# Optimization experiments

Measured on AMD Instinct MI355X. Metric: run time of the kernel, lower is better.

Reference implementation:

```python
import jax, jax.numpy as jnp
import numpy as np

B = 16384
OUT = 128          # output_size (per conditioning frame)
NCOND = 3
HID = 32           # MLP3 hidden
LSTM_H = 64        # lstm_output_size (input == hidden)
NPRED = 25
EPS = 1e-5


def setup_inputs() -> dict:
    key = jax.random.key(0)
    ks = jax.random.split(key, 20)
    d = {
        "x0": jax.random.normal(ks[0], (B, OUT), jnp.float32),
        "x1": jax.random.normal(ks[1], (B, OUT), jnp.float32),
        "x2": jax.random.normal(ks[2], (B, OUT), jnp.float32),
        # MLP3: Linear(384->32), BN, ReLU, Linear(32->32), BN, ReLU, Linear(32->64)
        "W1": jax.random.normal(ks[3], (HID, OUT * NCOND), jnp.float32) * 0.05,
        "b1": jnp.full((HID,), 0.03, jnp.float32),
        "g1": jnp.ones((HID,), jnp.float32),
        "beta1": jnp.zeros((HID,), jnp.float32),
        "W2": jax.random.normal(ks[4], (HID, HID), jnp.float32) * 0.1,
        "b2": jnp.full((HID,), 0.03, jnp.float32),
        "g2": jnp.ones((HID,), jnp.float32),
        "beta2": jnp.zeros((HID,), jnp.float32),
        "W3": jax.random.normal(ks[5], (LSTM_H, HID), jnp.float32) * 0.1,
        "b3": jnp.full((LSTM_H,), 0.03, jnp.float32),
        # LSTM (torch gate order i,f,g,o): weight_ih (4H,H), weight_hh (4H,H)
        "Wih": jax.random.normal(ks[6], (4 * LSTM_H, LSTM_H), jnp.float32) * 0.08,
        "Whh": jax.random.normal(ks[7], (4 * LSTM_H, LSTM_H), jnp.float32) * 0.08,
        "bih": jnp.zeros((4 * LSTM_H,), jnp.float32),
        "bhh": jnp.zeros((4 * LSTM_H,), jnp.float32),
    }
    return d


def _bn_train(h, g, b):
    # BatchNorm1d in training mode: biased batch statistics
    m = jnp.mean(h, axis=0)
    v = jnp.var(h, axis=0)
    return g * (h - m) * jax.lax.rsqrt(v + EPS) + b


def _lstm_step(inp, h, c, Wih, Whh, bih, bhh):
    gates = inp @ Wih.T + bih + h @ Whh.T + bhh  # (B, 4H)
    i, f, g, o = jnp.split(gates, 4, axis=1)
    c_new = jax.nn.sigmoid(f) * c + jax.nn.sigmoid(i) * jnp.tanh(g)
    h_new = jax.nn.sigmoid(o) * jnp.tanh(c_new)
    return h_new, c_new


def reference(x0, x1, x2, W1, b1, g1, beta1, W2, b2, g2, beta2, W3, b3,
              Wih, Whh, bih, bhh):
    x = jnp.concatenate([x0, x1, x2], axis=1)          # (B, 384)
    h = jax.nn.relu(_bn_train(x @ W1.T + b1, g1, beta1))
    h = jax.nn.relu(_bn_train(h @ W2.T + b2, g2, beta2))
    m = h @ W3.T + b3                                   # (B, 64)

    h0 = jnp.zeros((m.shape[0], LSTM_H), m.dtype)
    c0 = jnp.zeros_like(h0)
    # initial conditioning step (output discarded except as state/next input)
    h1, c1 = _lstm_step(m, h0, c0, Wih, Whh, bih, bhh)

    def step(carry, _):
        hh, cc = carry
        # loop feeds previous output back as input; output == h for 1-layer LSTM
        hn, cn = _lstm_step(hh, hh, cc, Wih, Whh, bih, bhh)
        return (hn, cn), hn

    _, outs = jax.lax.scan(step, (h1, c1), None, length=NPRED)  # (25, B, 64)
    return jnp.transpose(outs, (1, 0, 2))                        # (B, 25, 64)
```

## Files before the change

### kernel.cpp

```cpp
#include <hip/hip_runtime.h>


#define EPSV 1e-5f
#define LOG2E 1.4426950408889634f
#define K2    2.8853900817779268f

typedef __attribute__((ext_vector_type(8))) short bf16x8;
typedef __attribute__((ext_vector_type(4))) float f32x4;

__device__ __forceinline__ float rcp_f(float x) { return __builtin_amdgcn_rcpf(x); }
__device__ __forceinline__ void split_bf16(float x, ushort& hi, ushort& lo) {
    unsigned xb = __builtin_bit_cast(unsigned, x);
    hi = (ushort)(xb >> 16);
    float hif = __builtin_bit_cast(float, xb & 0xffff0000u);
    unsigned lb = __builtin_bit_cast(unsigned, x - hif);
    lo = (ushort)(lb >> 16);
}

__global__ __launch_bounds__(256) void k_prep(
    const float* __restrict__ Wih, const float* __restrict__ Whh,
    const float* __restrict__ bih, const float* __restrict__ bhh,
    const float* __restrict__ W1, const float* __restrict__ W2,
    ushort* __restrict__ Wih_hi, ushort* __restrict__ Wih_lo,
    ushort* __restrict__ Wsum_hi, ushort* __restrict__ Wsum_lo,
    ushort* __restrict__ W1hi, ushort* __restrict__ W1lo,
    ushort* __restrict__ W2hi, ushort* __restrict__ W2lo,
    float* __restrict__ bsum)
{
    int i = blockIdx.x * 256 + threadIdx.x;
    ushort h, l;
    if (i < 16384) {
        int j = i >> 6;
        float sc = (j >= 128 && j < 192) ? K2 : LOG2E;
        float wi  = Wih[i] * sc;
        float wsv = (Wih[i] + Whh[i]) * sc;
        split_bf16(wi, h, l);  Wih_hi[i] = h;  Wih_lo[i] = l;
        split_bf16(wsv, h, l); Wsum_hi[i] = h; Wsum_lo[i] = l;
    }
    if (i < 12288) { split_bf16(W1[i], h, l); W1hi[i] = h; W1lo[i] = l; }
    if (i < 1024)  { split_bf16(W2[i], h, l); W2hi[i] = h; W2lo[i] = l; }
    if (i < 256) {
        float sc = (i >= 128 && i < 192) ? K2 : LOG2E;
        bsum[i] = (bih[i] + bhh[i]) * sc;
    }
}

__global__ __launch_bounds__(256) void k_red(const float* __restrict__ part,
                                             const float* __restrict__ g,
                                             const float* __restrict__ be,
                                             float* __restrict__ scsh) {
    __shared__ float rs[256], rq[256];
    const int ch = blockIdx.x, t = threadIdx.x;
    float s = (part[t * 32 + ch] + part[(t + 256) * 32 + ch]) +
              (part[(t + 512) * 32 + ch] + part[(t + 768) * 32 + ch]);
    float q = (part[32768 + t * 32 + ch] + part[32768 + (t + 256) * 32 + ch]) +
              (part[32768 + (t + 512) * 32 + ch] + part[32768 + (t + 768) * 32 + ch]);
    rs[t] = s; rq[t] = q;
    __syncthreads();
    #pragma unroll
    for (int off = 128; off > 0; off >>= 1) {
        if (t < off) { rs[t] += rs[t + off]; rq[t] += rq[t + off]; }
        __syncthreads();
    }
    if (t == 0) {
        float mu = rs[0] * (1.f / 16384.f);
        float va = rq[0] * (1.f / 16384.f) - mu * mu;
        float sc = g[ch] * rsqrtf(va + EPSV);
        scsh[ch] = sc; scsh[32 + ch] = be[ch] - mu * sc;
    }
}

__global__ __launch_bounds__(256) void k_mlp1(
    const float* __restrict__ x0, const float* __restrict__ x1, const float* __restrict__ x2,
    const ushort* __restrict__ W1hi, const ushort* __restrict__ W1lo,
    const float* __restrict__ b1,
    float* __restrict__ pre, float* __restrict__ st1p)
{
    __shared__ __align__(16) ushort xhi[32 * 392];
    __shared__ __align__(16) ushort xlo[32 * 392];
    const int tid = threadIdx.x;
    const int r0  = blockIdx.x * 32;

    for (int a = 0; a < 3; ++a) {
        const float* xp = (a == 0) ? x0 : (a == 1) ? x1 : x2;
        const float4* src = (const float4*)(xp + (size_t)r0 * 128);
        #pragma unroll
        for (int it = 0; it < 4; ++it) {
            int i = it * 256 + tid;
            int row = i >> 5, c4 = i & 31;
            float4 v = src[i];
            ushort h0, l0, h1, l1, h2, l2, h3, l3;
            split_bf16(v.x, h0, l0); split_bf16(v.y, h1, l1);
            split_bf16(v.z, h2, l2); split_bf16(v.w, h3, l3);
            int ofs = row * 392 + a * 128 + c4 * 4;
            *(ushort4*)&xhi[ofs] = make_ushort4(h0, h1, h2, h3);
            *(ushort4*)&xlo[ofs] = make_ushort4(l0, l1, l2, l3);
        }
    }
    __syncthreads();

    const int lane = tid & 63, l15 = lane & 15, lg = lane >> 4, q = tid >> 6;
    const int m0 = (q & 1) * 16, n0 = (q >> 1) * 16;
    const float bias = b1[n0 + l15];
    f32x4 acc = {bias, bias, bias, bias};
    #pragma unroll
    for (int kt = 0; kt < 12; ++kt) {
        bf16x8 ahi = *(const bf16x8*)&xhi[(m0 + l15) * 392 + kt * 32 + lg * 8];
        bf16x8 alo = *(const bf16x8*)&xlo[(m0 + l15) * 392 + kt * 32 + lg * 8];
        bf16x8 bhi = *(const bf16x8*)(W1hi + (size_t)(n0 + l15) * 384 + kt * 32 + lg * 8);
        bf16x8 blo = *(const bf16x8*)(W1lo + (size_t)(n0 + l15) * 384 + kt * 32 + lg * 8);
        acc = __builtin_amdgcn_mfma_f32_16x16x32_bf16(ahi, bhi, acc, 0, 0, 0);
        acc = __builtin_amdgcn_mfma_f32_16x16x32_bf16(ahi, blo, acc, 0, 0, 0);
        acc = __builtin_amdgcn_mfma_f32_16x16x32_bf16(alo, bhi, acc, 0, 0, 0);
    }
    #pragma unroll
    for (int rg = 0; rg < 4; ++rg)
        pre[(size_t)(r0 + m0 + lg * 4 + rg) * 32 + n0 + l15] = acc[rg];
    float s  = (acc[0] + acc[1]) + (acc[2] + acc[3]);
    float sq = (acc[0] * acc[0] + acc[1] * acc[1]) + (acc[2] * acc[2] + acc[3] * acc[3]);
    s  += __shfl_xor(s, 16);  s  += __shfl_xor(s, 32);
    sq += __shfl_xor(sq, 16); sq += __shfl_xor(sq, 32);
    if (lg == 0) {
        int slot = (blockIdx.x * 2 + (q & 1)) * 32 + n0 + l15;
        st1p[slot] = s;
        st1p[32768 + slot] = sq;
    }
}

__global__ __launch_bounds__(256) void k_mlp2(
    float* __restrict__ pre, const float* __restrict__ scsh1,
    const ushort* __restrict__ W2hi, const ushort* __restrict__ W2lo,
    const float* __restrict__ b2, float* __restrict__ st2p)
{
    __shared__ __align__(16) ushort hhi[32 * 40];
    __shared__ __align__(16) ushort hlo[32 * 40];
    __shared__ float bnsc[32], bnsh[32];
    const int tid = threadIdx.x;
    const int r0  = blockIdx.x * 32;

    if (tid < 32) { bnsc[tid] = scsh1[tid]; bnsh[tid] = scsh1[32 + tid]; }
    __syncthreads();
    {
        int row = tid >> 3, c4 = tid & 7;
        float4 v = ((const float4*)(pre + (size_t)r0 * 32))[tid];
        float e0 = fmaxf(fmaf(v.x, bnsc[c4 * 4 + 0], bnsh[c4 * 4 + 0]), 0.f);
        float e1 = fmaxf(fmaf(v.y, bnsc[c4 * 4 + 1], bnsh[c4 * 4 + 1]), 0.f);
        float e2 = fmaxf(fmaf(v.z, bnsc[c4 * 4 + 2], bnsh[c4 * 4 + 2]), 0.f);
        float e3 = fmaxf(fmaf(v.w, bnsc[c4 * 4 + 3], bnsh[c4 * 4 + 3]), 0.f);
        ushort h0, l0, h1, l1, h2, l2, h3, l3;
        split_bf16(e0, h0, l0); split_bf16(e1, h1, l1);
        split_bf16(e2, h2, l2); split_bf16(e3, h3, l3);
        int ofs = row * 40 + c4 * 4;
        *(ushort4*)&hhi[ofs] = make_ushort4(h0, h1, h2, h3);
        *(ushort4*)&hlo[ofs] = make_ushort4(l0, l1, l2, l3);
    }
    __syncthreads();

    const int lane = tid & 63, l15 = lane & 15, lg = lane >> 4, q = tid >> 6;
    const int m0 = (q & 1) * 16, n0 = (q >> 1) * 16;
    const float bias = b2[n0 + l15];
    f32x4 acc = {bias, bias, bias, bias};
    bf16x8 ahi = *(const bf16x8*)&hhi[(m0 + l15) * 40 + lg * 8];
    bf16x8 alo = *(const bf16x8*)&hlo[(m0 + l15) * 40 + lg * 8];
    bf16x8 bhi = *(const bf16x8*)(W2hi + (size_t)(n0 + l15) * 32 + lg * 8);
    bf16x8 blo = *(const bf16x8*)(W2lo + (size_t)(n0 + l15) * 32 + lg * 8);
    acc = __builtin_amdgcn_mfma_f32_16x16x32_bf16(ahi, bhi, acc, 0, 0, 0);
    acc = __builtin_amdgcn_mfma_f32_16x16x32_bf16(ahi, blo, acc, 0, 0, 0);
    acc = __builtin_amdgcn_mfma_f32_16x16x32_bf16(alo, bhi, acc, 0, 0, 0);

    #pragma unroll
    for (int rg = 0; rg < 4; ++rg)
        pre[(size_t)(r0 + m0 + lg * 4 + rg) * 32 + n0 + l15] = acc[rg];
    float s  = (acc[0] + acc[1]) + (acc[2] + acc[3]);
    float sq = (acc[0] * acc[0] + acc[1] * acc[1]) + (acc[2] * acc[2] + acc[3] * acc[3]);
    s  += __shfl_xor(s, 16);  s  += __shfl_xor(s, 32);
    sq += __shfl_xor(sq, 16); sq += __shfl_xor(sq, 32);
    if (lg == 0) {
        int slot = (blockIdx.x * 2 + (q & 1)) * 32 + n0 + l15;
        st2p[slot] = s;
        st2p[32768 + slot] = sq;
    }
}

__global__ __launch_bounds__(256, 2) void k_lstm(
    const float* __restrict__ pre, const float* __restrict__ scsh2,
    const float* __restrict__ W3, const float* __restrict__ b3,
    const ushort* __restrict__ Wih_hi, const ushort* __restrict__ Wih_lo,
    const ushort* __restrict__ Wsum_hi, const ushort* __restrict__ Wsum_lo,
    const float* __restrict__ bsum, float* __restrict__ out)
{
    __shared__ __align__(16) ushort hhi[2][2][16][72];
    __shared__ __align__(16) ushort hlo[2][2][16][72];
    __shared__ float bn2sc[32], bn2sh[32];
    const int tid  = threadIdx.x;
    const int lane = tid & 63, l15 = lane & 15, lg = lane >> 4, q = tid >> 6;
    const int r0   = blockIdx.x * 32;

    if (tid < 32) { bn2sc[tid] = scsh2[tid]; bn2sh[tid] = scsh2[32 + tid]; }
    __syncthreads();

    {
        const int row = tid & 31, seg = tid >> 5;
        float h2[32];
        const float4* pr = (const float4*)(pre + (size_t)(r0 + row) * 32);
        #pragma unroll
        for (int j4 = 0; j4 < 8; ++j4) {
            float4 v = pr[j4];
            h2[j4 * 4 + 0] = v.x; h2[j4 * 4 + 1] = v.y;
            h2[j4 * 4 + 2] = v.z; h2[j4 * 4 + 3] = v.w;
        }
        #pragma unroll
        for (int j = 0; j < 32; ++j) h2[j] = fmaxf(fmaf(h2[j], bn2sc[j], bn2sh[j]), 0.f);
        #pragma unroll
        for (int uu = 0; uu < 8; ++uu) {
            int u = seg * 8 + uu;
            const float* w = W3 + u * 32;
            float a0 = 0.f, a1 = 0.f, a2 = 0.f, a3 = 0.f;
            #pragma unroll
            for (int k = 0; k < 32; k += 4) {
                a0 = fmaf(h2[k + 0], w[k + 0], a0);
                a1 = fmaf(h2[k + 1], w[k + 1], a1);
                a2 = fmaf(h2[k + 2], w[k + 2], a2);
                a3 = fmaf(h2[k + 3], w[k + 3], a3);
            }
            float m = b3[u] + ((a0 + a1) + (a2 + a3));
            ushort mh, ml; split_bf16(m, mh, ml);
            hhi[row >> 4][0][row & 15][u] = mh;
            hlo[row >> 4][0][row & 15][u] = ml;
        }
    }

    float bias[4];
    #pragma unroll
    for (int nt = 0; nt < 4; ++nt) bias[nt] = bsum[nt * 64 + q * 16 + l15];
    float cA[4] = {0.f, 0.f, 0.f, 0.f}, cB[4] = {0.f, 0.f, 0.f, 0.f};

    float* obA[4];
    float* obB[4];
    #pragma unroll
    for (int rg = 0; rg < 4; ++rg) {
        obA[rg] = out + (size_t)(r0 + lg * 4 + rg) * 1600 + (q * 16 + l15);
        obB[rg] = out + (size_t)(r0 + 16 + lg * 4 + rg) * 1600 + (q * 16 + l15);
    }

    bf16x8 Bhi[4][2], Blo[4][2];
    const size_t wofs = (size_t)(q * 16 + l15) * 64 + lg * 8;
    #pragma unroll
    for (int nt = 0; nt < 4; ++nt)
        #pragma unroll
        for (int kt = 0; kt < 2; ++kt) {
            Bhi[nt][kt] = *(const bf16x8*)(Wih_hi + (size_t)nt * 4096 + wofs + kt * 32);
            Blo[nt][kt] = *(const bf16x8*)(Wih_lo + (size_t)nt * 4096 + wofs + kt * 32);
        }
    __syncthreads();

#define MFMA_GATES(ACC, G, BUF)                                                  \
    {                                                                            \
        _Pragma("unroll")                                                        \
        for (int nt = 0; nt < 4; ++nt)                                           \
            ACC[nt] = (f32x4){bias[nt], bias[nt], bias[nt], bias[nt]};           \
        _Pragma("unroll")                                                        \
        for (int kt = 0; kt < 2; ++kt) {                                         \
            bf16x8 ahi = *(const bf16x8*)&hhi[G][BUF][l15][kt * 32 + lg * 8];    \
            bf16x8 alo = *(const bf16x8*)&hlo[G][BUF][l15][kt * 32 + lg * 8];    \
            _Pragma("unroll")                                                    \
            for (int nt = 0; nt < 4; ++nt) {                                     \
                ACC[nt] = __builtin_amdgcn_mfma_f32_16x16x32_bf16(ahi, Bhi[nt][kt], ACC[nt], 0, 0, 0); \
                ACC[nt] = __builtin_amdgcn_mfma_f32_16x16x32_bf16(ahi, Blo[nt][kt], ACC[nt], 0, 0, 0); \
                ACC[nt] = __builtin_amdgcn_mfma_f32_16x16x32_bf16(alo, Bhi[nt][kt], ACC[nt], 0, 0, 0); \
            }                                                                    \
        }                                                                        \
    }

#define ACT(ACC, C, G, WBUF, OB, SLOT, WRST)                                     \
    {                                                                            \
        const int u = q * 16 + l15;                                              \
        _Pragma("unroll")                                                        \
        for (int rg = 0; rg < 4; ++rg) {                                         \
            int row = lg * 4 + rg;                                               \
            float iv = ACC[0][rg], fv = ACC[1][rg];                              \
            float gv = ACC[2][rg], ov = ACC[3][rg];                              \
            float Af = __builtin_amdgcn_exp2f(-fv);                              \
            float Ai = __builtin_amdgcn_exp2f(-iv);                              \
            float Bg = __builtin_amdgcn_exp2f(gv);                               \
            float sig = (Bg - 1.f) * rcp_f((1.f + Ai) * (Bg + 1.f));             \
            float cc = C[rg] * rcp_f(1.f + Af) + sig;                            \
            C[rg] = cc;                                                          \
            float Ao = __builtin_amdgcn_exp2f(-ov);                              \
            float C2 = __builtin_amdgcn_exp2f(cc * K2);                          \
            float hn = (C2 - 1.f) * rcp_f((1.f + Ao) * (C2 + 1.f));              \
            ushort hh, hl; split_bf16(hn, hh, hl);                               \
            hhi[G][WBUF][row][u] = hh;                                           \
            hlo[G][WBUF][row][u] = hl;                                           \
            if (WRST)                                                            \
                OB[rg][(size_t)(SLOT) * 64] = hn;                                \
        }                                                                        \
    }

    f32x4 accA[4], accB[4];

    MFMA_GATES(accA, 0, 0);
    MFMA_GATES(accB, 1, 0);
    #pragma unroll
    for (int nt = 0; nt < 4; ++nt)
        #pragma unroll
        for (int kt = 0; kt < 2; ++kt) {
            Bhi[nt][kt] = *(const bf16x8*)(Wsum_hi + (size_t)nt * 4096 + wofs + kt * 32);
            Blo[nt][kt] = *(const bf16x8*)(Wsum_lo + (size_t)nt * 4096 + wofs + kt * 32);
        }
    ACT(accA, cA, 0, 1, obA, 0, 0);
    ACT(accB, cB, 1, 1, obB, 0, 0);
    __syncthreads();

    #pragma unroll 1
    for (int s = 1; s <= 25; ++s) {
        const int rb = s & 1, wb = rb ^ 1;
        MFMA_GATES(accA, 0, rb);
        MFMA_GATES(accB, 1, rb);
        ACT(accA, cA, 0, wb, obA, s - 1, 1);
        ACT(accB, cB, 1, wb, obB, s - 1, 1);
        __syncthreads();
    }

#undef MFMA_GATES
#undef ACT
}

extern "C" void kernel_launch(void* const* d_in, const int* in_sizes, int n_in,
                              void* d_out, int out_size, void* d_ws, size_t ws_size,
                              hipStream_t stream) {
    const float* x0   = (const float*)d_in[0];
    const float* x1   = (const float*)d_in[1];
    const float* x2   = (const float*)d_in[2];
    const float* W1   = (const float*)d_in[3];
    const float* b1   = (const float*)d_in[4];
    const float* g1   = (const float*)d_in[5];
    const float* be1  = (const float*)d_in[6];
    const float* W2   = (const float*)d_in[7];
    const float* b2   = (const float*)d_in[8];
    const float* g2   = (const float*)d_in[9];
    const float* be2  = (const float*)d_in[10];
    const float* W3   = (const float*)d_in[11];
    const float* b3   = (const float*)d_in[12];
    const float* Wih  = (const float*)d_in[13];
    const float* Whh  = (const float*)d_in[14];
    const float* bih  = (const float*)d_in[15];
    const float* bhh  = (const float*)d_in[16];

    float* ws    = (float*)d_ws;
    float* pre   = ws;
    float* st1p  = ws + 524288;
    float* st2p  = ws + 589824;
    float* scsh1 = ws + 655360;
    float* scsh2 = ws + 655424;
    float* bsum  = ws + 655488;
    ushort* ub   = (ushort*)(ws + 655744);
    ushort* Wih_hi  = ub;
    ushort* Wih_lo  = ub + 16384;
    ushort* Wsum_hi = ub + 32768;
    ushort* Wsum_lo = ub + 49152;
    ushort* W1hi    = ub + 65536;
    ushort* W1lo    = ub + 77824;
    ushort* W2hi    = ub + 90112;
    ushort* W2lo    = ub + 91136;

    hipLaunchKernelGGL(k_prep, dim3(64), dim3(256), 0, stream,
                       Wih, Whh, bih, bhh, W1, W2,
                       Wih_hi, Wih_lo, Wsum_hi, Wsum_lo, W1hi, W1lo, W2hi, W2lo, bsum);
    hipLaunchKernelGGL(k_mlp1, dim3(512), dim3(256), 0, stream,
                       x0, x1, x2, W1hi, W1lo, b1, pre, st1p);
    hipLaunchKernelGGL(k_red, dim3(32), dim3(256), 0, stream, st1p, g1, be1, scsh1);
    hipLaunchKernelGGL(k_mlp2, dim3(512), dim3(256), 0, stream,
                       pre, scsh1, W2hi, W2lo, b2, st2p);
    hipLaunchKernelGGL(k_red, dim3(32), dim3(256), 0, stream, st2p, g2, be2, scsh2);
    hipLaunchKernelGGL(k_lstm, dim3(512), dim3(256), 0, stream,
                       pre, scsh2, W3, b3,
                       Wih_hi, Wih_lo, Wsum_hi, Wsum_lo, bsum, (float*)d_out);
}
```

Measured before the change: 87.45 us.

## Eliminate prep kernel: split MLP weights in-kernel, fold LSTM prep into reduction

Removes the standalone weight-prep launch. k_mlp1 and k_mlp2 now load the fp32 W1/W2 directly and split them into bf16 hi/lo register fragments inside each block. The LSTM weight split moves into the first k_red launch. k_mlp1 also gets a launch bound of 2 waves per SIMD. Separately, k_lstm makes the upper half of its blocks s_sleep once before the recurrence, apparently to stagger memory or issue contention. The trade is one fewer launch against redundant per-block splitting of W1, higher register pressure, and a deliberate stall in half the LSTM blocks.

```diff
diff --git a/kernel.cpp b/kernel.cpp
--- a/kernel.cpp
+++ b/kernel.cpp
@@ -16,41 +16,45 @@
     unsigned lb = __builtin_bit_cast(unsigned, x - hif);
     lo = (ushort)(lb >> 16);
 }
-
-__global__ __launch_bounds__(256) void k_prep(
+__device__ __forceinline__ void split8(const float* w, bf16x8& hiv, bf16x8& lov) {
+    ushort hs[8], ls[8];
+    #pragma unroll
+    for (int j = 0; j < 8; ++j) split_bf16(w[j], hs[j], ls[j]);
+    hiv = *(bf16x8*)hs;
+    lov = *(bf16x8*)ls;
+}
+
+__global__ __launch_bounds__(256) void k_red(
+    const float* __restrict__ part, const float* __restrict__ g,
+    const float* __restrict__ be, float* __restrict__ scsh,
+    int do_prep,
     const float* __restrict__ Wih, const float* __restrict__ Whh,
     const float* __restrict__ bih, const float* __restrict__ bhh,
-    const float* __restrict__ W1, const float* __restrict__ W2,
     ushort* __restrict__ Wih_hi, ushort* __restrict__ Wih_lo,
     ushort* __restrict__ Wsum_hi, ushort* __restrict__ Wsum_lo,
-    ushort* __restrict__ W1hi, ushort* __restrict__ W1lo,
-    ushort* __restrict__ W2hi, ushort* __restrict__ W2lo,
     float* __restrict__ bsum)
 {
-    int i = blockIdx.x * 256 + threadIdx.x;
-    ushort h, l;
-    if (i < 16384) {
-        int j = i >> 6;
-        float sc = (j >= 128 && j < 192) ? K2 : LOG2E;
-        float wi  = Wih[i] * sc;
-        float wsv = (Wih[i] + Whh[i]) * sc;
-        split_bf16(wi, h, l);  Wih_hi[i] = h;  Wih_lo[i] = l;
-        split_bf16(wsv, h, l); Wsum_hi[i] = h; Wsum_lo[i] = l;
-    }
-    if (i < 12288) { split_bf16(W1[i], h, l); W1hi[i] = h; W1lo[i] = l; }
-    if (i < 1024)  { split_bf16(W2[i], h, l); W2hi[i] = h; W2lo[i] = l; }
-    if (i < 256) {
-        float sc = (i >= 128 && i < 192) ? K2 : LOG2E;
-        bsum[i] = (bih[i] + bhh[i]) * sc;
-    }
-}
-
-__global__ __launch_bounds__(256) void k_red(const float* __restrict__ part,
-                                             const float* __restrict__ g,
-                                             const float* __restrict__ be,
-                                             float* __restrict__ scsh) {
     __shared__ float rs[256], rq[256];
     const int ch = blockIdx.x, t = threadIdx.x;
+
+    if (do_prep) {
+        #pragma unroll
+        for (int e = 0; e < 2; ++e) {
+            int i = blockIdx.x * 512 + e * 256 + t;
+            int j = i >> 6;
+            float sc = (j >= 128 && j < 192) ? K2 : LOG2E;
+            float wi  = Wih[i] * sc;
+            float wsv = (Wih[i] + Whh[i]) * sc;
+            ushort h, l;
+            split_bf16(wi, h, l);  Wih_hi[i] = h;  Wih_lo[i] = l;
+            split_bf16(wsv, h, l); Wsum_hi[i] = h; Wsum_lo[i] = l;
+        }
+        if (blockIdx.x == 0) {
+            float sc = (t >= 128 && t < 192) ? K2 : LOG2E;
+            bsum[t] = (bih[t] + bhh[t]) * sc;
+        }
+    }
+
     float s = (part[t * 32 + ch] + part[(t + 256) * 32 + ch]) +
               (part[(t + 512) * 32 + ch] + part[(t + 768) * 32 + ch]);
     float q = (part[32768 + t * 32 + ch] + part[32768 + (t + 256) * 32 + ch]) +
@@ -70,16 +74,31 @@
     }
 }
 
-__global__ __launch_bounds__(256) void k_mlp1(
+__global__ __launch_bounds__(256, 2) void k_mlp1(
     const float* __restrict__ x0, const float* __restrict__ x1, const float* __restrict__ x2,
-    const ushort* __restrict__ W1hi, const ushort* __restrict__ W1lo,
-    const float* __restrict__ b1,
+    const float* __restrict__ W1, const float* __restrict__ b1,
     float* __restrict__ pre, float* __restrict__ st1p)
 {
     __shared__ __align__(16) ushort xhi[32 * 392];
     __shared__ __align__(16) ushort xlo[32 * 392];
     const int tid = threadIdx.x;
     const int r0  = blockIdx.x * 32;
+    const int lane = tid & 63, l15 = lane & 15, lg = lane >> 4, q = tid >> 6;
+    const int m0 = (q & 1) * 16, n0 = (q >> 1) * 16;
+
+    bf16x8 WH[12], WL[12];
+    {
+        const float* wsrc = W1 + (size_t)(n0 + l15) * 384 + lg * 8;
+        #pragma unroll
+        for (int kt = 0; kt < 12; ++kt) {
+            float w[8];
+            float4 wa = *(const float4*)(wsrc + kt * 32);
+            float4 wb = *(const float4*)(wsrc + kt * 32 + 4);
+            w[0] = wa.x; w[1] = wa.y; w[2] = wa.z; w[3] = wa.w;
+            w[4] = wb.x; w[5] = wb.y; w[6] = wb.z; w[7] = wb.w;
+            split8(w, WH[kt], WL[kt]);
+        }
+    }
 
     for (int a = 0; a < 3; ++a) {
         const float* xp = (a == 0) ? x0 : (a == 1) ? x1 : x2;
@@ -99,19 +118,15 @@
     }
     __syncthreads();
 
-    const int lane = tid & 63, l15 = lane & 15, lg = lane >> 4, q = tid >> 6;
-    const int m0 = (q & 1) * 16, n0 = (q >> 1) * 16;
     const float bias = b1[n0 + l15];
     f32x4 acc = {bias, bias, bias, bias};
     #pragma unroll
     for (int kt = 0; kt < 12; ++kt) {
         bf16x8 ahi = *(const bf16x8*)&xhi[(m0 + l15) * 392 + kt * 32 + lg * 8];
         bf16x8 alo = *(const bf16x8*)&xlo[(m0 + l15) * 392 + kt * 32 + lg * 8];
-        bf16x8 bhi = *(const bf16x8*)(W1hi + (size_t)(n0 + l15) * 384 + kt * 32 + lg * 8);
-        bf16x8 blo = *(const bf16x8*)(W1lo + (size_t)(n0 + l15) * 384 + kt * 32 + lg * 8);
-        acc = __builtin_amdgcn_mfma_f32_16x16x32_bf16(ahi, bhi, acc, 0, 0, 0);
-        acc = __builtin_amdgcn_mfma_f32_16x16x32_bf16(ahi, blo, acc, 0, 0, 0);
-        acc = __builtin_amdgcn_mfma_f32_16x16x32_bf16(alo, bhi, acc, 0, 0, 0);
+        acc = __builtin_amdgcn_mfma_f32_16x16x32_bf16(ahi, WH[kt], acc, 0, 0, 0);
+        acc = __builtin_amdgcn_mfma_f32_16x16x32_bf16(ahi, WL[kt], acc, 0, 0, 0);
+        acc = __builtin_amdgcn_mfma_f32_16x16x32_bf16(alo, WH[kt], acc, 0, 0, 0);
     }
     #pragma unroll
     for (int rg = 0; rg < 4; ++rg)
@@ -129,14 +144,27 @@
 
 __global__ __launch_bounds__(256) void k_mlp2(
     float* __restrict__ pre, const float* __restrict__ scsh1,
-    const ushort* __restrict__ W2hi, const ushort* __restrict__ W2lo,
-    const float* __restrict__ b2, float* __restrict__ st2p)
+    const float* __restrict__ W2, const float* __restrict__ b2,
+    float* __restrict__ st2p)
 {
     __shared__ __align__(16) ushort hhi[32 * 40];
     __shared__ __align__(16) ushort hlo[32 * 40];
     __shared__ float bnsc[32], bnsh[32];
     const int tid = threadIdx.x;
     const int r0  = blockIdx.x * 32;
+    const int lane = tid & 63, l15 = lane & 15, lg = lane >> 4, q = tid >> 6;
+    const int m0 = (q & 1) * 16, n0 = (q >> 1) * 16;
+
+    bf16x8 W2H, W2L;
+    {
+        const float* wsrc = W2 + (size_t)(n0 + l15) * 32 + lg * 8;
+        float w[8];
+        float4 wa = *(const float4*)(wsrc);
+        float4 wb = *(const float4*)(wsrc + 4);
+        w[0] = wa.x; w[1] = wa.y; w[2] = wa.z; w[3] = wa.w;
+        w[4] = wb.x; w[5] = wb.y; w[6] = wb.z; w[7] = wb.w;
+        split8(w, W2H, W2L);
+    }
 
     if (tid < 32) { bnsc[tid] = scsh1[tid]; bnsh[tid] = scsh1[32 + tid]; }
     __syncthreads();
@@ -156,17 +184,13 @@
     }
     __syncthreads();
 
-    const int lane = tid & 63, l15 = lane & 15, lg = lane >> 4, q = tid >> 6;
-    const int m0 = (q & 1) * 16, n0 = (q >> 1) * 16;
     const float bias = b2[n0 + l15];
     f32x4 acc = {bias, bias, bias, bias};
     bf16x8 ahi = *(const bf16x8*)&hhi[(m0 + l15) * 40 + lg * 8];
     bf16x8 alo = *(const bf16x8*)&hlo[(m0 + l15) * 40 + lg * 8];
-    bf16x8 bhi = *(const bf16x8*)(W2hi + (size_t)(n0 + l15) * 32 + lg * 8);
-    bf16x8 blo = *(const bf16x8*)(W2lo + (size_t)(n0 + l15) * 32 + lg * 8);
-    acc = __builtin_amdgcn_mfma_f32_16x16x32_bf16(ahi, bhi, acc, 0, 0, 0);
-    acc = __builtin_amdgcn_mfma_f32_16x16x32_bf16(ahi, blo, acc, 0, 0, 0);
-    acc = __builtin_amdgcn_mfma_f32_16x16x32_bf16(alo, bhi, acc, 0, 0, 0);
+    acc = __builtin_amdgcn_mfma_f32_16x16x32_bf16(ahi, W2H, acc, 0, 0, 0);
+    acc = __builtin_amdgcn_mfma_f32_16x16x32_bf16(ahi, W2L, acc, 0, 0, 0);
+    acc = __builtin_amdgcn_mfma_f32_16x16x32_bf16(alo, W2H, acc, 0, 0, 0);
 
     #pragma unroll
     for (int rg = 0; rg < 4; ++rg)
@@ -253,6 +277,8 @@
             Blo[nt][kt] = *(const bf16x8*)(Wih_lo + (size_t)nt * 4096 + wofs + kt * 32);
         }
     __syncthreads();
+
+    if ((blockIdx.x >> 8) & 1) __builtin_amdgcn_s_sleep(46);
 
 #define MFMA_GATES(ACC, G, BUF)                                                  \
     {                                                                            \
@@ -359,20 +385,17 @@
     ushort* Wih_lo  = ub + 16384;
     ushort* Wsum_hi = ub + 32768;
     ushort* Wsum_lo = ub + 49152;
-    ushort* W1hi    = ub + 65536;
-    ushort* W1lo    = ub + 77824;
-    ushort* W2hi    = ub + 90112;
-    ushort* W2lo    = ub + 91136;
-
-    hipLaunchKernelGGL(k_prep, dim3(64), dim3(256), 0, stream,
-                       Wih, Whh, bih, bhh, W1, W2,
-                       Wih_hi, Wih_lo, Wsum_hi, Wsum_lo, W1hi, W1lo, W2hi, W2lo, bsum);
+
     hipLaunchKernelGGL(k_mlp1, dim3(512), dim3(256), 0, stream,
-                       x0, x1, x2, W1hi, W1lo, b1, pre, st1p);
-    hipLaunchKernelGGL(k_red, dim3(32), dim3(256), 0, stream, st1p, g1, be1, scsh1);
+                       x0, x1, x2, W1, b1, pre, st1p);
+    hipLaunchKernelGGL(k_red, dim3(32), dim3(256), 0, stream,
+                       st1p, g1, be1, scsh1,
+                       1, Wih, Whh, bih, bhh, Wih_hi, Wih_lo, Wsum_hi, Wsum_lo, bsum);
     hipLaunchKernelGGL(k_mlp2, dim3(512), dim3(256), 0, stream,
-                       pre, scsh1, W2hi, W2lo, b2, st2p);
-    hipLaunchKernelGGL(k_red, dim3(32), dim3(256), 0, stream, st2p, g2, be2, scsh2);
+                       pre, scsh1, W2, b2, st2p);
+    hipLaunchKernelGGL(k_red, dim3(32), dim3(256), 0, stream,
+                       st2p, g2, be2, scsh2,
+                       0, Wih, Whh, bih, bhh, Wih_hi, Wih_lo, Wsum_hi, Wsum_lo, bsum);
     hipLaunchKernelGGL(k_lstm, dim3(512), dim3(256), 0, stream,
                        pre, scsh2, W3, b3,
                        Wih_hi, Wih_lo, Wsum_hi, Wsum_lo, bsum, (float*)d_out);
```

After: 82.08 us. 1.07x faster.
